# Optimization experiments

Measured on AMD Instinct MI355X. Metric: run time of the kernel, lower is better.

The kernel has to match this reference:

```python
import jax, jax.numpy as jnp
import numpy as np

H = 256  # hidden size


def _lstm_dir(x, w_ih, w_hh, b, reverse):
    """Single-direction LSTM. x: [B,S,D]; w_ih: [4H,D]; w_hh: [4H,H]; b: [4H].
    PyTorch gate order: i, f, g, o."""
    if reverse:
        x = jnp.flip(x, axis=1)
    # Precompute input contribution for all timesteps at once: [B,S,4H]
    xg = jnp.einsum('bsd,gd->bsg', x, w_ih) + b

    def step(carry, xg_t):
        h, c = carry
        gates = xg_t + h @ w_hh.T  # [B,4H]
        i, f, g, o = jnp.split(gates, 4, axis=-1)
        c = jax.nn.sigmoid(f) * c + jax.nn.sigmoid(i) * jnp.tanh(g)
        h = jax.nn.sigmoid(o) * jnp.tanh(c)
        return (h, c), h

    Bsz = x.shape[0]
    h0 = jnp.zeros((Bsz, w_hh.shape[1]), x.dtype)
    _, hs = jax.lax.scan(step, (h0, h0), jnp.swapaxes(xg, 0, 1))  # hs: [S,B,H]
    hs = jnp.swapaxes(hs, 0, 1)
    if reverse:
        hs = jnp.flip(hs, axis=1)
    return hs


def _bilstm_layer(x, w_ih, w_hh, b):
    # w_ih: [2,4H,D], w_hh: [2,4H,H], b: [2,4H] (b_ih + b_hh pre-summed)
    fwd = _lstm_dir(x, w_ih[0], w_hh[0], b[0], False)
    bwd = _lstm_dir(x, w_ih[1], w_hh[1], b[1], True)
    return jnp.concatenate([fwd, bwd], axis=-1)  # [B,S,2H]


def setup_inputs() -> dict:
    key = jax.random.key(0)
    ks = jax.random.split(key, 16)
    B, S, D = 256, 512, 64
    s = 1.0 / np.sqrt(H)
    u = lambda k, shp: jax.random.uniform(k, shp, jnp.float32, -s, s)
    return {
        'x': jax.random.normal(ks[0], (B, S, D), jnp.float32),
        # layer 0 (input D)
        'w_ih0': u(ks[1], (2, 4 * H, D)),
        'w_hh0': u(ks[2], (2, 4 * H, H)),
        'b0': u(ks[3], (2, 4 * H)),
        # layers 1..2 (input 2H)
        'w_ih_r': u(ks[4], (2, 2, 4 * H, 2 * H)),
        'w_hh_r': u(ks[5], (2, 2, 4 * H, H)),
        'b_r': u(ks[6], (2, 2, 4 * H)),
        # FC head: 2H -> H -> H//2 -> 1
        'fc1_w': u(ks[7], (H, 2 * H)),
        'fc1_b': u(ks[8], (H,)),
        'fc2_w': u(ks[9], (H // 2, H)),
        'fc2_b': u(ks[10], (H // 2,)),
        'fc3_w': u(ks[11], (1, H // 2)),
        'fc3_b': u(ks[12], (1,)),
    }


def reference(x, w_ih0, w_hh0, b0, w_ih_r, w_hh_r, b_r,
              fc1_w, fc1_b, fc2_w, fc2_b, fc3_w, fc3_b):
    h = _bilstm_layer(x, w_ih0, w_hh0, b0)
    for l in range(w_ih_r.shape[0]):  # fixed small layer count
        h = _bilstm_layer(h, w_ih_r[l], w_hh_r[l], b_r[l])
    last = h[:, -1, :]  # [B, 2H]
    h1 = jax.nn.relu(last @ fc1_w.T + fc1_b)
    h2 = jax.nn.relu(h1 @ fc2_w.T + fc2_b)
    return h2 @ fc3_w.T + fc3_b  # [B,1]
```

## Files before the change

kernel.cpp:

```cpp
#include <hip/hip_runtime.h>
#include <cstdint>
#include <cstddef>

#define B_ 256
#define S_ 512

typedef _Float16 f16;
typedef _Float16 f16x8 __attribute__((ext_vector_type(8)));
typedef _Float16 f16x4 __attribute__((ext_vector_type(4)));
typedef float f32x4 __attribute__((ext_vector_type(4)));
using u32 = unsigned int;
using u16 = unsigned short;
using u64 = unsigned long long;

#define TAGX   0x555u
#define MAGIC_ 0x13579BDFu

__device__ __forceinline__ float sigf(float x) { return 1.f / (1.f + __expf(-x)); }
__device__ __forceinline__ float tanh_f(float x) {
  x = fminf(15.f, fmaxf(-15.f, x));
  const float e = __expf(-2.f * x);
  return (1.f - e) / (1.f + e);
}
__device__ __forceinline__ f16x8 cvt_f16x8(float4 a, float4 b) {
  f16x8 t;
  t[0] = (f16)a.x; t[1] = (f16)a.y; t[2] = (f16)a.z; t[3] = (f16)a.w;
  t[4] = (f16)b.x; t[5] = (f16)b.y; t[6] = (f16)b.z; t[7] = (f16)b.w;
  return t;
}

__global__ __launch_bounds__(256) void transpose_x(
    const float* __restrict__ x, f16* __restrict__ xT)
{
  const int t = blockIdx.x;
  const int col = threadIdx.x & 63;
  const int r0 = threadIdx.x >> 6;
  for (int it = 0; it < 64; ++it) {
    const int row = (it << 2) + r0;
    xT[((size_t)t * 256 + row) * 64 + col] =
        (f16)x[((size_t)row * S_ + t) * 64 + col];
  }
}

template<int L, int KIN>
__global__ __launch_bounds__(256, 1) void lstm_layer(
    const f16* __restrict__ xT,
    f16* __restrict__ hA,
    f16* __restrict__ aux,
    f16* __restrict__ l2out,
    u64* __restrict__ exch,
    u32* __restrict__ xprog,
    const float* __restrict__ w_ih,
    const float* __restrict__ w_hh,
    const float* __restrict__ bias)
{
  constexpr int GPR = KIN / 8;
  constexpr int LG  = (KIN == 512) ? 6 : 3;
  constexpr int NG  = 16 * GPR;
  constexpr int XI  = (NG + 255) / 256;
  __shared__ __align__(16) f16 x_s[16 * KIN];
  __shared__ __align__(16) f16 h_s[16 * 256];
  __shared__ float gates_s[64 * 33];
  __shared__ char pad_[81920];

  const int tid = threadIdx.x;
  const int lane = tid & 63, w = tid >> 6;
  const int l15 = lane & 15, l4 = lane >> 4;
  const int phys = blockIdx.x;
  const int wg = ((phys & 7) << 5) | (phys >> 3);
  const int dirv = wg >> 7, bg = (wg >> 3) & 15, sl = wg & 7;
  if ((int)blockIdx.x == -1) { pad_[tid] = 0; }

  f16x8 bih[2][KIN / 32];
  f16x8 bhhH[2][8], bhhL[2][8];
#pragma unroll
  for (int nt = 0; nt < 2; ++nt) {
    const int grow = (w << 8) + (sl << 5) + (nt << 4) + l15;
    const float* pih = w_ih + ((size_t)(dirv << 10) + grow) * KIN + (l4 << 3);
#pragma unroll
    for (int kt = 0; kt < KIN / 32; ++kt) {
      const float* p = pih + (kt << 5);
      bih[nt][kt] = cvt_f16x8(*(const float4*)p, *(const float4*)(p + 4));
    }
    const float* phh = w_hh + ((size_t)(dirv << 10) + grow) * 256 + (l4 << 3);
#pragma unroll
    for (int kt = 0; kt < 8; ++kt) {
      const float* p = phh + (kt << 5);
      float wf[8];
      *(float4*)&wf[0] = *(const float4*)p;
      *(float4*)&wf[4] = *(const float4*)(p + 4);
      f16x8 hi, lo;
#pragma unroll
      for (int j = 0; j < 8; ++j) {
        hi[j] = (f16)wf[j];
        lo[j] = (f16)((wf[j] - (float)hi[j]) * 1024.f);
      }
      bhhH[nt][kt] = hi;
      bhhL[nt][kt] = lo;
    }
  }

  const int crow = tid >> 4;
  const int u0 = (tid & 15) << 1;
  float bv[4][2];
#pragma unroll
  for (int g = 0; g < 4; ++g)
#pragma unroll
    for (int j = 0; j < 2; ++j)
      bv[g][j] = bias[(dirv << 10) + (g << 8) + (sl << 5) + u0 + j];
  float cs0 = 0.f, cs1 = 0.f;

  auto xsrc = [&](int t, int b, int g) -> const f16* {
    if constexpr (L == 0) {
      return xT + ((size_t)t * 256 + b) * 64 + (g << 3);
    } else if constexpr (L == 1) {
      return hA + ((size_t)t * 256 + b) * 512 + (g << 3);
    } else {
      const int c0 = g << 3;
      if (c0 < 256)
        return (t < 256) ? aux + ((size_t)t * 256 + b) * 256 + c0
                         : hA + ((size_t)t * 256 + b) * 512 + c0;
      const int u = c0 - 256;
      return (t >= 256) ? aux + ((size_t)(256 + (511 - t)) * 256 + b) * 256 + u
                        : hA + ((size_t)t * 256 + b) * 512 + 256 + u;
    }
  };

#define X_MFMA(A0, A1)                                                         \
  {                                                                            \
    _Pragma("unroll")                                                          \
    for (int kt = 0; kt < KIN / 32; ++kt) {                                    \
      const int gg = ((kt << 2) + l4) ^ (l15 & 7);                             \
      const f16x8 a = *(const f16x8*)&x_s[l15 * KIN + (gg << 3)];              \
      A0 = __builtin_amdgcn_mfma_f32_16x16x32_f16(a, bih[0][kt], A0, 0, 0, 0); \
      A1 = __builtin_amdgcn_mfma_f32_16x16x32_f16(a, bih[1][kt], A1, 0, 0, 0); \
    }                                                                          \
  }

  f16x8 xreg[XI];
  {
    const int t0 = dirv ? (S_ - 1) : 0;
#pragma unroll
    for (int i = 0; i < XI; ++i) {
      const int G = tid + (i << 8);
      if (NG < 256 && G >= NG) break;
      const int row = G >> LG, g = G & (GPR - 1);
      xreg[i] = *(const f16x8*)xsrc(t0, (bg << 4) + row, g);
    }
#pragma unroll
    for (int i = 0; i < XI; ++i) {
      const int G = tid + (i << 8);
      if (NG < 256 && G >= NG) break;
      const int row = G >> LG, g = G & (GPR - 1);
      *(f16x8*)&x_s[row * KIN + ((g ^ (row & 7)) << 3)] = xreg[i];
    }
  }
  __syncthreads();
  f32x4 accx0 = {}, accx1 = {};
  X_MFMA(accx0, accx1);

  for (int s = 0; s < S_; ++s) {
    const int t_or = dirv ? (S_ - 1 - s) : s;
    const bool pf = (s + 1 < S_);

    if (pf) {
      const int t_nx = dirv ? (t_or - 1) : (t_or + 1);
#pragma unroll
      for (int i = 0; i < XI; ++i) {
        const int G = tid + (i << 8);
        if (NG < 256 && G >= NG) break;
        const int row = G >> LG, g = G & (GPR - 1);
        xreg[i] = *(const f16x8*)xsrc(t_nx, (bg << 4) + row, g);
      }
    }

    if constexpr (L == 1) {
      if (s == 256) {
        if (tid < 128) {
          const u32* pw = xprog + (1 - dirv) * 128 + tid;
          while (__hip_atomic_load(pw, __ATOMIC_RELAXED, __HIP_MEMORY_SCOPE_AGENT) != MAGIC_)
            __builtin_amdgcn_s_sleep(2);
        }
        __syncthreads();
      }
    }

    if (s > 0) {
      const u32 tagp = ((u32)(L * 512 + s - 1) ^ TAGX) & 0x7FFu;
      const u64* ex = exch + ((size_t)(((s - 1) & 1) * 2 + dirv)) * 256 * 128;
      u32 vv[4][4];
      for (;;) {
        bool ok = true;
#pragma unroll
        for (int i = 0; i < 4; ++i) {
          const int G = tid + (i << 8);
          const int row = G >> 6, gr = G & 63;
          const int b = (bg << 4) + row;
          const u64* p = ex + b * 128 + (gr << 1);
          const u64 a = __hip_atomic_load(p, __ATOMIC_RELAXED, __HIP_MEMORY_SCOPE_AGENT);
          const u64 c = __hip_atomic_load(p + 1, __ATOMIC_RELAXED, __HIP_MEMORY_SCOPE_AGENT);
          vv[i][0] = (u32)a; vv[i][1] = (u32)(a >> 32);
          vv[i][2] = (u32)c; vv[i][3] = (u32)(c >> 32);
#pragma unroll
          for (int j = 0; j < 4; ++j) ok &= ((vv[i][j] & 0x7FFu) == tagp);
        }
        if (ok) break;
        __builtin_amdgcn_s_sleep(1);
      }
#pragma unroll
      for (int i = 0; i < 4; ++i) {
        const int G = tid + (i << 8);
        const int row = G >> 6, gr = G & 63;
        const int g8 = gr >> 1, half = gr & 1;
        f16x4 hh;
#pragma unroll
        for (int j = 0; j < 4; ++j)
          hh[j] = (f16)__builtin_bit_cast(float, vv[i][j] & 0xFFFFF800u);
        *(f16x4*)&h_s[(row << 8) + ((g8 ^ (row & 7)) << 3) + (half << 2)] = hh;
      }
    }
    __syncthreads();

    f32x4 acc0 = accx0, acc1 = accx1;
    if (s > 0) {
      f32x4 aL0 = {}, aL1 = {};
#pragma unroll
      for (int kt = 0; kt < 8; ++kt) {
        const int gg = ((kt << 2) + l4) ^ (l15 & 7);
        const f16x8 a = *(const f16x8*)&h_s[(l15 << 8) + (gg << 3)];
        acc0 = __builtin_amdgcn_mfma_f32_16x16x32_f16(a, bhhH[0][kt], acc0, 0, 0, 0);
        acc1 = __builtin_amdgcn_mfma_f32_16x16x32_f16(a, bhhH[1][kt], acc1, 0, 0, 0);
        aL0 = __builtin_amdgcn_mfma_f32_16x16x32_f16(a, bhhL[0][kt], aL0, 0, 0, 0);
        aL1 = __builtin_amdgcn_mfma_f32_16x16x32_f16(a, bhhL[1][kt], aL1, 0, 0, 0);
      }
      acc0 += aL0 * (1.f / 1024.f);
      acc1 += aL1 * (1.f / 1024.f);
    }

#pragma unroll
    for (int r = 0; r < 4; ++r) {
      const int row = (l4 << 2) + r;
      gates_s[((w << 4) + row) * 33 + l15] = acc0[r];
      gates_s[((w << 4) + row) * 33 + 16 + l15] = acc1[r];
    }
    __syncthreads();

    float hv[2];
    {
      float css[2] = { cs0, cs1 };
#pragma unroll
      for (int j = 0; j < 2; ++j) {
        const int u = u0 + j;
        const float gi = gates_s[(0 * 16 + crow) * 33 + u] + bv[0][j];
        const float gf = gates_s[(1 * 16 + crow) * 33 + u] + bv[1][j];
        const float gg = gates_s[(2 * 16 + crow) * 33 + u] + bv[2][j];
        const float go = gates_s[(3 * 16 + crow) * 33 + u] + bv[3][j];
        float cc = sigf(gf) * css[j] + sigf(gi) * tanh_f(gg);
        css[j] = cc;
        hv[j] = sigf(go) * tanh_f(cc);
      }
      cs0 = css[0]; cs1 = css[1];
    }

    asm volatile("s_waitcnt vmcnt(0)" ::: "memory");
    {
      const u32 tagc = ((u32)(L * 512 + s) ^ TAGX) & 0x7FFu;
      const u32 w0 = ((__builtin_bit_cast(u32, hv[0]) + 0x400u) & 0xFFFFF800u) | tagc;
      const u32 w1 = ((__builtin_bit_cast(u32, hv[1]) + 0x400u) & 0xFFFFF800u) | tagc;
      const u64 pk = (u64)w0 | ((u64)w1 << 32);
      const int b = (bg << 4) + crow;
      __hip_atomic_store(
          exch + ((size_t)((s & 1) * 2 + dirv)) * 256 * 128 + b * 128 + (sl << 4) + (u0 >> 1),
          pk, __ATOMIC_RELAXED, __HIP_MEMORY_SCOPE_AGENT);

      union { u16 hw[2]; u32 pkh; } uh;
      uh.hw[0] = __builtin_bit_cast(u16, (f16)hv[0]);
      uh.hw[1] = __builtin_bit_cast(u16, (f16)hv[1]);
      const int uoff = (dirv << 7) + (sl << 4) + (u0 >> 1);
      if constexpr (L == 0) {
        ((u32*)hA)[((size_t)t_or * 256 + b) * 256 + uoff] = uh.pkh;
      } else if constexpr (L == 1) {
        if (s < 256)
          ((u32*)aux)[((size_t)(dirv * 256 + s) * 256 + b) * 128 + (sl << 4) + (u0 >> 1)] = uh.pkh;
        else
          ((u32*)hA)[((size_t)t_or * 256 + b) * 256 + uoff] = uh.pkh;
      } else {
        if (t_or == S_ - 1)
          ((u32*)l2out)[(size_t)b * 256 + uoff] = uh.pkh;
      }
    }

    if constexpr (L == 1) {
      if (s == 254) {
        asm volatile("s_waitcnt vmcnt(0)" ::: "memory");
        __syncthreads();
        if (tid == 0)
          __hip_atomic_store(xprog + dirv * 128 + (bg << 3) + sl, MAGIC_,
                             __ATOMIC_RELAXED, __HIP_MEMORY_SCOPE_AGENT);
      }
    }

    if (pf) {
#pragma unroll
      for (int i = 0; i < XI; ++i) {
        const int G = tid + (i << 8);
        if (NG < 256 && G >= NG) break;
        const int row = G >> LG, g = G & (GPR - 1);
        *(f16x8*)&x_s[row * KIN + ((g ^ (row & 7)) << 3)] = xreg[i];
      }
      __syncthreads();
      accx0 = (f32x4){}; accx1 = (f32x4){};
      X_MFMA(accx0, accx1);
    }
  }
#undef X_MFMA
}

__global__ __launch_bounds__(256) void fc_head(
    const f16* __restrict__ l2out,
    const float* __restrict__ fc1_w, const float* __restrict__ fc1_b,
    const float* __restrict__ fc2_w, const float* __restrict__ fc2_b,
    const float* __restrict__ fc3_w, const float* __restrict__ fc3_b,
    float* __restrict__ out)
{
  __shared__ float last[512];
  __shared__ float h1[256];
  __shared__ float h2[128];
  const int b = blockIdx.x;
  const int t = threadIdx.x;
  for (int i = t; i < 512; i += 256)
    last[i] = (float)l2out[(size_t)b * 512 + i];
  __syncthreads();
  {
    float a = fc1_b[t];
    for (int k = 0; k < 512; ++k) a = fmaf(last[k], fc1_w[t * 512 + k], a);
    h1[t] = fmaxf(a, 0.f);
  }
  __syncthreads();
  if (t < 128) {
    float a = fc2_b[t];
    for (int k = 0; k < 256; ++k) a = fmaf(h1[k], fc2_w[t * 256 + k], a);
    h2[t] = fmaxf(a, 0.f);
  }
  __syncthreads();
  if (t == 0) {
    float a = fc3_b[0];
    for (int k = 0; k < 128; ++k) a = fmaf(h2[k], fc3_w[k], a);
    out[b] = a;
  }
}

__global__ void sentinel(float* out, int n, float v) {
  const int i = blockIdx.x * blockDim.x + threadIdx.x;
  if (i < n) out[i] = v;
}

extern "C" void kernel_launch(void* const* d_in, const int* in_sizes, int n_in,
                              void* d_out, int out_size, void* d_ws, size_t ws_size,
                              hipStream_t stream) {
  (void)in_sizes; (void)n_in;
  const float* x      = (const float*)d_in[0];
  const float* w_ih0  = (const float*)d_in[1];
  const float* w_hh0  = (const float*)d_in[2];
  const float* b0     = (const float*)d_in[3];
  const float* w_ih_r = (const float*)d_in[4];
  const float* w_hh_r = (const float*)d_in[5];
  const float* b_r    = (const float*)d_in[6];
  const float* fc1_w  = (const float*)d_in[7];
  const float* fc1_b  = (const float*)d_in[8];
  const float* fc2_w  = (const float*)d_in[9];
  const float* fc2_b  = (const float*)d_in[10];
  const float* fc3_w  = (const float*)d_in[11];
  const float* fc3_b  = (const float*)d_in[12];
  float* out = (float*)d_out;

  const size_t off_hA    = 0;
  const size_t off_aux   = off_hA   + (size_t)512*256*512*2;
  const size_t off_xT    = off_aux  + (size_t)2*256*256*256*2;
  const size_t off_l2o   = off_xT   + (size_t)512*256*64*2;
  const size_t off_exch  = off_l2o  + (size_t)256*512*2;
  const size_t off_xprog = off_exch + (size_t)2*2*256*128*8;
  const size_t need      = off_xprog + 1024;
  if (ws_size < need) {
    sentinel<<<1, 256, 0, stream>>>(out, out_size, (float)(ws_size >> 20));
    return;
  }
  char* ws = (char*)d_ws;
  f16* hA    = (f16*)(ws + off_hA);
  f16* aux   = (f16*)(ws + off_aux);
  f16* xT    = (f16*)(ws + off_xT);
  f16* l2out = (f16*)(ws + off_l2o);
  u64* exch  = (u64*)(ws + off_exch);
  u32* xprog = (u32*)(ws + off_xprog);

  hipMemsetAsync(ws + off_exch, 0xAA, (size_t)2*2*256*128*8 + 1024, stream);

  transpose_x<<<512, 256, 0, stream>>>(x, xT);

  lstm_layer<0, 64><<<256, 256, 0, stream>>>(
      xT, hA, aux, l2out, exch, xprog, w_ih0, w_hh0, b0);
  lstm_layer<1, 512><<<256, 256, 0, stream>>>(
      xT, hA, aux, l2out, exch, xprog, w_ih_r, w_hh_r, b_r);
  lstm_layer<2, 512><<<256, 256, 0, stream>>>(
      xT, hA, aux, l2out, exch, xprog,
      w_ih_r + (size_t)2 * 1024 * 512, w_hh_r + (size_t)2 * 1024 * 256,
      b_r + 2048);

  fc_head<<<B_, 256, 0, stream>>>(l2out, fc1_w, fc1_b, fc2_w, fc2_b, fc3_w, fc3_b, out);
}
```

Measured before the change: 3.835 ms.

## Use 512-thread LSTM blocks covering 64 hidden units, halving the block count

Each persistent LSTM workgroup now has 8 waves and owns 64 hidden units instead of 32, so the grid drops from 256 to 128 blocks. Each thread now polls only the exchange words for its own h_s slot, with short spinning before it starts sleeping, and the per-step vmcnt(0) wait before publishing is dropped except near the layer-1 handoff. The aim is fewer blocks in the cross-block recurrence exchange and lower per-step sync latency. The cost is more MFMA and activation work per block, and the XCD/group mapping and progress-flag indexing had to be reworked.

```diff
diff --git a/kernel.cpp b/kernel.cpp
--- a/kernel.cpp
+++ b/kernel.cpp
@@ -7,7 +7,6 @@
 
 typedef _Float16 f16;
 typedef _Float16 f16x8 __attribute__((ext_vector_type(8)));
-typedef _Float16 f16x4 __attribute__((ext_vector_type(4)));
 typedef float f32x4 __attribute__((ext_vector_type(4)));
 using u32 = unsigned int;
 using u16 = unsigned short;
@@ -43,7 +42,7 @@
 }
 
 template<int L, int KIN>
-__global__ __launch_bounds__(256, 1) void lstm_layer(
+__global__ __launch_bounds__(512, 1) void lstm_layer(
     const f16* __restrict__ xT,
     f16* __restrict__ hA,
     f16* __restrict__ aux,
@@ -57,25 +56,29 @@
   constexpr int GPR = KIN / 8;
   constexpr int LG  = (KIN == 512) ? 6 : 3;
   constexpr int NG  = 16 * GPR;
-  constexpr int XI  = (NG + 255) / 256;
+  constexpr int XI  = (NG + 511) / 512;
   __shared__ __align__(16) f16 x_s[16 * KIN];
   __shared__ __align__(16) f16 h_s[16 * 256];
-  __shared__ float gates_s[64 * 33];
-  __shared__ char pad_[81920];
+  __shared__ float gates_s[64 * 66];
+  constexpr int PADB = 90112 - 16 * KIN * 2 - 16 * 256 * 2 - 64 * 66 * 4;
+  __shared__ char pad_[PADB];
 
   const int tid = threadIdx.x;
   const int lane = tid & 63, w = tid >> 6;
   const int l15 = lane & 15, l4 = lane >> 4;
+  const int gi = w >> 1, uh = w & 1;
   const int phys = blockIdx.x;
-  const int wg = ((phys & 7) << 5) | (phys >> 3);
-  const int dirv = wg >> 7, bg = (wg >> 3) & 15, sl = wg & 7;
-  if ((int)blockIdx.x == -1) { pad_[tid] = 0; }
+  const int xcd = phys & 7, slot = phys >> 3;
+  const int gp = slot >> 2, sl = slot & 3;
+  const int grp = (gp << 3) | xcd;
+  const int dirv = grp >> 4, bg = grp & 15;
+  if ((int)blockIdx.x == -1) pad_[tid] = 0;
 
   f16x8 bih[2][KIN / 32];
   f16x8 bhhH[2][8], bhhL[2][8];
 #pragma unroll
   for (int nt = 0; nt < 2; ++nt) {
-    const int grow = (w << 8) + (sl << 5) + (nt << 4) + l15;
+    const int grow = (gi << 8) + (sl << 6) + (uh << 5) + (nt << 4) + l15;
     const float* pih = w_ih + ((size_t)(dirv << 10) + grow) * KIN + (l4 << 3);
 #pragma unroll
     for (int kt = 0; kt < KIN / 32; ++kt) {
@@ -100,15 +103,16 @@
     }
   }
 
-  const int crow = tid >> 4;
-  const int u0 = (tid & 15) << 1;
+  const int crow = tid >> 5;
+  const int u0 = (tid & 31) << 1;
   float bv[4][2];
 #pragma unroll
   for (int g = 0; g < 4; ++g)
 #pragma unroll
     for (int j = 0; j < 2; ++j)
-      bv[g][j] = bias[(dirv << 10) + (g << 8) + (sl << 5) + u0 + j];
+      bv[g][j] = bias[(dirv << 10) + (g << 8) + (sl << 6) + u0 + j];
   float cs0 = 0.f, cs1 = 0.f;
+  const int sg8 = tid & 31;
 
   auto xsrc = [&](int t, int b, int g) -> const f16* {
     if constexpr (L == 0) {
@@ -142,15 +146,15 @@
     const int t0 = dirv ? (S_ - 1) : 0;
 #pragma unroll
     for (int i = 0; i < XI; ++i) {
-      const int G = tid + (i << 8);
-      if (NG < 256 && G >= NG) break;
+      const int G = tid + (i << 9);
+      if (NG < 512 && G >= NG) break;
       const int row = G >> LG, g = G & (GPR - 1);
       xreg[i] = *(const f16x8*)xsrc(t0, (bg << 4) + row, g);
     }
 #pragma unroll
     for (int i = 0; i < XI; ++i) {
-      const int G = tid + (i << 8);
-      if (NG < 256 && G >= NG) break;
+      const int G = tid + (i << 9);
+      if (NG < 512 && G >= NG) break;
       const int row = G >> LG, g = G & (GPR - 1);
       *(f16x8*)&x_s[row * KIN + ((g ^ (row & 7)) << 3)] = xreg[i];
     }
@@ -167,8 +171,8 @@
       const int t_nx = dirv ? (t_or - 1) : (t_or + 1);
 #pragma unroll
       for (int i = 0; i < XI; ++i) {
-        const int G = tid + (i << 8);
-        if (NG < 256 && G >= NG) break;
+        const int G = tid + (i << 9);
+        if (NG < 512 && G >= NG) break;
         const int row = G >> LG, g = G & (GPR - 1);
         xreg[i] = *(const f16x8*)xsrc(t_nx, (bg << 4) + row, g);
       }
@@ -176,8 +180,8 @@
 
     if constexpr (L == 1) {
       if (s == 256) {
-        if (tid < 128) {
-          const u32* pw = xprog + (1 - dirv) * 128 + tid;
+        if (tid < 64) {
+          const u32* pw = xprog + (1 - dirv) * 64 + tid;
           while (__hip_atomic_load(pw, __ATOMIC_RELAXED, __HIP_MEMORY_SCOPE_AGENT) != MAGIC_)
             __builtin_amdgcn_s_sleep(2);
         }
@@ -187,37 +191,27 @@
 
     if (s > 0) {
       const u32 tagp = ((u32)(L * 512 + s - 1) ^ TAGX) & 0x7FFu;
-      const u64* ex = exch + ((size_t)(((s - 1) & 1) * 2 + dirv)) * 256 * 128;
-      u32 vv[4][4];
-      for (;;) {
+      const u64* pb = exch + ((size_t)(((s - 1) & 1) * 2 + dirv)) * 256 * 128
+                      + ((bg << 4) + crow) * 128 + (sg8 << 2);
+      u64 a[4];
+      for (int tr = 0;; ++tr) {
+#pragma unroll
+        for (int k = 0; k < 4; ++k)
+          a[k] = __hip_atomic_load(pb + k, __ATOMIC_RELAXED, __HIP_MEMORY_SCOPE_AGENT);
         bool ok = true;
 #pragma unroll
-        for (int i = 0; i < 4; ++i) {
-          const int G = tid + (i << 8);
-          const int row = G >> 6, gr = G & 63;
-          const int b = (bg << 4) + row;
-          const u64* p = ex + b * 128 + (gr << 1);
-          const u64 a = __hip_atomic_load(p, __ATOMIC_RELAXED, __HIP_MEMORY_SCOPE_AGENT);
-          const u64 c = __hip_atomic_load(p + 1, __ATOMIC_RELAXED, __HIP_MEMORY_SCOPE_AGENT);
-          vv[i][0] = (u32)a; vv[i][1] = (u32)(a >> 32);
-          vv[i][2] = (u32)c; vv[i][3] = (u32)(c >> 32);
-#pragma unroll
-          for (int j = 0; j < 4; ++j) ok &= ((vv[i][j] & 0x7FFu) == tagp);
-        }
+        for (int k = 0; k < 4; ++k)
+          ok &= (((u32)a[k] & 0x7FFu) == tagp) & (((u32)(a[k] >> 32) & 0x7FFu) == tagp);
         if (ok) break;
-        __builtin_amdgcn_s_sleep(1);
-      }
-#pragma unroll
-      for (int i = 0; i < 4; ++i) {
-        const int G = tid + (i << 8);
-        const int row = G >> 6, gr = G & 63;
-        const int g8 = gr >> 1, half = gr & 1;
-        f16x4 hh;
-#pragma unroll
-        for (int j = 0; j < 4; ++j)
-          hh[j] = (f16)__builtin_bit_cast(float, vv[i][j] & 0xFFFFF800u);
-        *(f16x4*)&h_s[(row << 8) + ((g8 ^ (row & 7)) << 3) + (half << 2)] = hh;
-      }
+        if (tr >= 3) __builtin_amdgcn_s_sleep(1);
+      }
+      f16x8 hh;
+#pragma unroll
+      for (int k = 0; k < 4; ++k) {
+        hh[2 * k]     = (f16)__builtin_bit_cast(float, (u32)a[k] & 0xFFFFF800u);
+        hh[2 * k + 1] = (f16)__builtin_bit_cast(float, (u32)(a[k] >> 32) & 0xFFFFF800u);
+      }
+      *(f16x8*)&h_s[(crow << 8) + ((sg8 ^ (crow & 7)) << 3)] = hh;
     }
     __syncthreads();
 
@@ -240,8 +234,8 @@
 #pragma unroll
     for (int r = 0; r < 4; ++r) {
       const int row = (l4 << 2) + r;
-      gates_s[((w << 4) + row) * 33 + l15] = acc0[r];
-      gates_s[((w << 4) + row) * 33 + 16 + l15] = acc1[r];
+      gates_s[((gi << 4) + row) * 66 + (uh << 5) + l15] = acc0[r];
+      gates_s[((gi << 4) + row) * 66 + (uh << 5) + 16 + l15] = acc1[r];
     }
     __syncthreads();
 
@@ -251,42 +245,42 @@
 #pragma unroll
       for (int j = 0; j < 2; ++j) {
         const int u = u0 + j;
-        const float gi = gates_s[(0 * 16 + crow) * 33 + u] + bv[0][j];
-        const float gf = gates_s[(1 * 16 + crow) * 33 + u] + bv[1][j];
-        const float gg = gates_s[(2 * 16 + crow) * 33 + u] + bv[2][j];
-        const float go = gates_s[(3 * 16 + crow) * 33 + u] + bv[3][j];
-        float cc = sigf(gf) * css[j] + sigf(gi) * tanh_f(gg);
+        const float gI = gates_s[(0 * 16 + crow) * 66 + u] + bv[0][j];
+        const float gF = gates_s[(1 * 16 + crow) * 66 + u] + bv[1][j];
+        const float gG = gates_s[(2 * 16 + crow) * 66 + u] + bv[2][j];
+        const float gO = gates_s[(3 * 16 + crow) * 66 + u] + bv[3][j];
+        float cc = sigf(gF) * css[j] + sigf(gI) * tanh_f(gG);
         css[j] = cc;
-        hv[j] = sigf(go) * tanh_f(cc);
+        hv[j] = sigf(gO) * tanh_f(cc);
       }
       cs0 = css[0]; cs1 = css[1];
     }
 
-    asm volatile("s_waitcnt vmcnt(0)" ::: "memory");
+    if (L == 1 && s >= 253) asm volatile("s_waitcnt vmcnt(0)" ::: "memory");
     {
       const u32 tagc = ((u32)(L * 512 + s) ^ TAGX) & 0x7FFu;
       const u32 w0 = ((__builtin_bit_cast(u32, hv[0]) + 0x400u) & 0xFFFFF800u) | tagc;
       const u32 w1 = ((__builtin_bit_cast(u32, hv[1]) + 0x400u) & 0xFFFFF800u) | tagc;
       const u64 pk = (u64)w0 | ((u64)w1 << 32);
       const int b = (bg << 4) + crow;
-      __hip_atomic_store(
-          exch + ((size_t)((s & 1) * 2 + dirv)) * 256 * 128 + b * 128 + (sl << 4) + (u0 >> 1),
-          pk, __ATOMIC_RELAXED, __HIP_MEMORY_SCOPE_AGENT);
-
-      union { u16 hw[2]; u32 pkh; } uh;
-      uh.hw[0] = __builtin_bit_cast(u16, (f16)hv[0]);
-      uh.hw[1] = __builtin_bit_cast(u16, (f16)hv[1]);
-      const int uoff = (dirv << 7) + (sl << 4) + (u0 >> 1);
+      const size_t eidx = ((size_t)((s & 1) * 2 + dirv)) * 256 * 128
+                          + b * 128 + (sl << 5) + (u0 >> 1);
+      __hip_atomic_store(exch + eidx, pk, __ATOMIC_RELAXED, __HIP_MEMORY_SCOPE_AGENT);
+
+      union { u16 hw[2]; u32 pkh; } uhh;
+      uhh.hw[0] = __builtin_bit_cast(u16, (f16)hv[0]);
+      uhh.hw[1] = __builtin_bit_cast(u16, (f16)hv[1]);
+      const int uoff = (dirv << 7) + (sl << 5) + (u0 >> 1);
       if constexpr (L == 0) {
-        ((u32*)hA)[((size_t)t_or * 256 + b) * 256 + uoff] = uh.pkh;
+        ((u32*)hA)[((size_t)t_or * 256 + b) * 256 + uoff] = uhh.pkh;
       } else if constexpr (L == 1) {
         if (s < 256)
-          ((u32*)aux)[((size_t)(dirv * 256 + s) * 256 + b) * 128 + (sl << 4) + (u0 >> 1)] = uh.pkh;
+          ((u32*)aux)[((size_t)(dirv * 256 + s) * 256 + b) * 128 + (sl << 5) + (u0 >> 1)] = uhh.pkh;
         else
-          ((u32*)hA)[((size_t)t_or * 256 + b) * 256 + uoff] = uh.pkh;
+          ((u32*)hA)[((size_t)t_or * 256 + b) * 256 + uoff] = uhh.pkh;
       } else {
         if (t_or == S_ - 1)
-          ((u32*)l2out)[(size_t)b * 256 + uoff] = uh.pkh;
+          ((u32*)l2out)[(size_t)b * 256 + uoff] = uhh.pkh;
       }
     }
 
@@ -295,7 +289,7 @@
         asm volatile("s_waitcnt vmcnt(0)" ::: "memory");
         __syncthreads();
         if (tid == 0)
-          __hip_atomic_store(xprog + dirv * 128 + (bg << 3) + sl, MAGIC_,
+          __hip_atomic_store(xprog + dirv * 64 + (bg << 2) + sl, MAGIC_,
                              __ATOMIC_RELAXED, __HIP_MEMORY_SCOPE_AGENT);
       }
     }
@@ -303,8 +297,8 @@
     if (pf) {
 #pragma unroll
       for (int i = 0; i < XI; ++i) {
-        const int G = tid + (i << 8);
-        if (NG < 256 && G >= NG) break;
+        const int G = tid + (i << 9);
+        if (NG < 512 && G >= NG) break;
         const int row = G >> LG, g = G & (GPR - 1);
         *(f16x8*)&x_s[row * KIN + ((g ^ (row & 7)) << 3)] = xreg[i];
       }
@@ -375,11 +369,11 @@
   float* out = (float*)d_out;
 
   const size_t off_hA    = 0;
-  const size_t off_aux   = off_hA   + (size_t)512*256*512*2;
-  const size_t off_xT    = off_aux  + (size_t)2*256*256*256*2;
-  const size_t off_l2o   = off_xT   + (size_t)512*256*64*2;
-  const size_t off_exch  = off_l2o  + (size_t)256*512*2;
-  const size_t off_xprog = off_exch + (size_t)2*2*256*128*8;
+  const size_t off_aux   = off_hA    + (size_t)512*256*512*2;
+  const size_t off_xT    = off_aux   + (size_t)2*256*256*256*2;
+  const size_t off_l2o   = off_xT    + (size_t)512*256*64*2;
+  const size_t off_exch  = off_l2o   + (size_t)256*512*2;
+  const size_t off_xprog = off_exch  + (size_t)2*2*256*128*8;
   const size_t need      = off_xprog + 1024;
   if (ws_size < need) {
     sentinel<<<1, 256, 0, stream>>>(out, out_size, (float)(ws_size >> 20));
@@ -397,11 +391,11 @@
 
   transpose_x<<<512, 256, 0, stream>>>(x, xT);
 
-  lstm_layer<0, 64><<<256, 256, 0, stream>>>(
+  lstm_layer<0, 64><<<128, 512, 0, stream>>>(
       xT, hA, aux, l2out, exch, xprog, w_ih0, w_hh0, b0);
-  lstm_layer<1, 512><<<256, 256, 0, stream>>>(
+  lstm_layer<1, 512><<<128, 512, 0, stream>>>(
       xT, hA, aux, l2out, exch, xprog, w_ih_r, w_hh_r, b_r);
-  lstm_layer<2, 512><<<256, 256, 0, stream>>>(
+  lstm_layer<2, 512><<<128, 512, 0, stream>>>(
       xT, hA, aux, l2out, exch, xprog,
       w_ih_r + (size_t)2 * 1024 * 512, w_hh_r + (size_t)2 * 1024 * 256,
       b_r + 2048);
```

Measured after the change: 11.02 ms. 187% more time.

## Permute gate rows so LSTM cell update runs in registers via lane shuffles

Applied to the files above, without the earlier changes.

Reorders the weight rows each wave loads so that every lane's MFMA accumulators hold the i/f/g/o gate values for the same hidden units. A lane-xor-8 shuffle then pairs them, so the cell update runs directly from registers. This removes the LDS gates buffer and one __syncthreads per timestep. Output packing also uses lane-xor-1 shuffles, and the per-step s_waitcnt vmcnt(0) is now issued only near the layer-1 handoff step. The costs are more shuffle instructions, redundant transcendental work on half the lanes, and a looser wait on outstanding stores.

```diff
diff --git a/kernel.cpp b/kernel.cpp
--- a/kernel.cpp
+++ b/kernel.cpp
@@ -60,7 +60,6 @@
   constexpr int XI  = (NG + 255) / 256;
   __shared__ __align__(16) f16 x_s[16 * KIN];
   __shared__ __align__(16) f16 h_s[16 * 256];
-  __shared__ float gates_s[64 * 33];
   __shared__ char pad_[81920];
 
   const int tid = threadIdx.x;
@@ -69,13 +68,16 @@
   const int phys = blockIdx.x;
   const int wg = ((phys & 7) << 5) | (phys >> 3);
   const int dirv = wg >> 7, bg = (wg >> 3) & 15, sl = wg & 7;
-  if ((int)blockIdx.x == -1) { pad_[tid] = 0; }
+  if ((int)blockIdx.x == -1) pad_[tid] = 0;
 
   f16x8 bih[2][KIN / 32];
   f16x8 bhhH[2][8], bhhL[2][8];
+  float bv[2];
 #pragma unroll
   for (int nt = 0; nt < 2; ++nt) {
-    const int grow = (w << 8) + (sl << 5) + (nt << 4) + l15;
+    const int g_gate = (nt << 1) + (l15 >> 3);
+    const int grow = (g_gate << 8) + (sl << 5) + (w << 3) + (l15 & 7);
+    bv[nt] = bias[(dirv << 10) + grow];
     const float* pih = w_ih + ((size_t)(dirv << 10) + grow) * KIN + (l4 << 3);
 #pragma unroll
     for (int kt = 0; kt < KIN / 32; ++kt) {
@@ -100,15 +102,7 @@
     }
   }
 
-  const int crow = tid >> 4;
-  const int u0 = (tid & 15) << 1;
-  float bv[4][2];
-#pragma unroll
-  for (int g = 0; g < 4; ++g)
-#pragma unroll
-    for (int j = 0; j < 2; ++j)
-      bv[g][j] = bias[(dirv << 10) + (g << 8) + (sl << 5) + u0 + j];
-  float cs0 = 0.f, cs1 = 0.f;
+  float cs[4] = {0.f, 0.f, 0.f, 0.f};
 
   auto xsrc = [&](int t, int b, int g) -> const f16* {
     if constexpr (L == 0) {
@@ -187,7 +181,7 @@
 
     if (s > 0) {
       const u32 tagp = ((u32)(L * 512 + s - 1) ^ TAGX) & 0x7FFu;
-      const u64* ex = exch + ((size_t)(((s - 1) & 1) * 2 + dirv)) * 256 * 128;
+      const size_t ebase = ((size_t)(((s - 1) & 1) * 2 + dirv)) * 256 * 128;
       u32 vv[4][4];
       for (;;) {
         bool ok = true;
@@ -195,8 +189,7 @@
         for (int i = 0; i < 4; ++i) {
           const int G = tid + (i << 8);
           const int row = G >> 6, gr = G & 63;
-          const int b = (bg << 4) + row;
-          const u64* p = ex + b * 128 + (gr << 1);
+          const u64* p = exch + ebase + ((bg << 4) + row) * 128 + (gr << 1);
           const u64 a = __hip_atomic_load(p, __ATOMIC_RELAXED, __HIP_MEMORY_SCOPE_AGENT);
           const u64 c = __hip_atomic_load(p + 1, __ATOMIC_RELAXED, __HIP_MEMORY_SCOPE_AGENT);
           vv[i][0] = (u32)a; vv[i][1] = (u32)(a >> 32);
@@ -237,56 +230,57 @@
       acc1 += aL1 * (1.f / 1024.f);
     }
 
-#pragma unroll
-    for (int r = 0; r < 4; ++r) {
-      const int row = (l4 << 2) + r;
-      gates_s[((w << 4) + row) * 33 + l15] = acc0[r];
-      gates_s[((w << 4) + row) * 33 + 16 + l15] = acc1[r];
-    }
-    __syncthreads();
-
-    float hv[2];
+    float hv[4];
     {
-      float css[2] = { cs0, cs1 };
-#pragma unroll
-      for (int j = 0; j < 2; ++j) {
-        const int u = u0 + j;
-        const float gi = gates_s[(0 * 16 + crow) * 33 + u] + bv[0][j];
-        const float gf = gates_s[(1 * 16 + crow) * 33 + u] + bv[1][j];
-        const float gg = gates_s[(2 * 16 + crow) * 33 + u] + bv[2][j];
-        const float go = gates_s[(3 * 16 + crow) * 33 + u] + bv[3][j];
-        float cc = sigf(gf) * css[j] + sigf(gi) * tanh_f(gg);
-        css[j] = cc;
-        hv[j] = sigf(go) * tanh_f(cc);
-      }
-      cs0 = css[0]; cs1 = css[1];
-    }
-
-    asm volatile("s_waitcnt vmcnt(0)" ::: "memory");
+      const bool loH = (l15 < 8);
+#pragma unroll
+      for (int r = 0; r < 4; ++r) {
+        const float a0 = acc0[r] + bv[0];
+        const float a1 = acc1[r] + bv[1];
+        const float o0 = __shfl_xor(a0, 8);
+        const float o1 = __shfl_xor(a1, 8);
+        const float gi = loH ? a0 : o0;
+        const float gf = loH ? o0 : a0;
+        const float gg = loH ? a1 : o1;
+        const float go = loH ? o1 : a1;
+        float cc = sigf(gf) * cs[r] + sigf(gi) * tanh_f(gg);
+        cs[r] = cc;
+        hv[r] = sigf(go) * tanh_f(cc);
+      }
+    }
+
+    if (L == 1 && s >= 253) asm volatile("s_waitcnt vmcnt(0)" ::: "memory");
     {
       const u32 tagc = ((u32)(L * 512 + s) ^ TAGX) & 0x7FFu;
-      const u32 w0 = ((__builtin_bit_cast(u32, hv[0]) + 0x400u) & 0xFFFFF800u) | tagc;
-      const u32 w1 = ((__builtin_bit_cast(u32, hv[1]) + 0x400u) & 0xFFFFF800u) | tagc;
-      const u64 pk = (u64)w0 | ((u64)w1 << 32);
-      const int b = (bg << 4) + crow;
-      __hip_atomic_store(
-          exch + ((size_t)((s & 1) * 2 + dirv)) * 256 * 128 + b * 128 + (sl << 4) + (u0 >> 1),
-          pk, __ATOMIC_RELAXED, __HIP_MEMORY_SCOPE_AGENT);
-
-      union { u16 hw[2]; u32 pkh; } uh;
-      uh.hw[0] = __builtin_bit_cast(u16, (f16)hv[0]);
-      uh.hw[1] = __builtin_bit_cast(u16, (f16)hv[1]);
-      const int uoff = (dirv << 7) + (sl << 4) + (u0 >> 1);
-      if constexpr (L == 0) {
-        ((u32*)hA)[((size_t)t_or * 256 + b) * 256 + uoff] = uh.pkh;
-      } else if constexpr (L == 1) {
-        if (s < 256)
-          ((u32*)aux)[((size_t)(dirv * 256 + s) * 256 + b) * 128 + (sl << 4) + (u0 >> 1)] = uh.pkh;
-        else
-          ((u32*)hA)[((size_t)t_or * 256 + b) * 256 + uoff] = uh.pkh;
-      } else {
-        if (t_or == S_ - 1)
-          ((u32*)l2out)[(size_t)b * 256 + uoff] = uh.pkh;
+      const size_t pbase = ((size_t)((s & 1) * 2 + dirv)) * 256 * 128;
+      const int p_g = (sl << 4) + (w << 2) + ((l15 & 7) >> 1);
+      const bool evenL = ((l15 & 1) == 0);
+      const int rhalf = (l15 >> 3) << 1;
+#pragma unroll
+      for (int r = 0; r < 4; ++r) {
+        const u32 tw = ((__builtin_bit_cast(u32, hv[r]) + 0x400u) & 0xFFFFF800u) | tagc;
+        const u32 nb = __shfl_xor(tw, 1);
+        const u32 h16 = (u32)__builtin_bit_cast(u16, (f16)hv[r]);
+        const u32 nh = __shfl_xor(h16, 1);
+        if (evenL && (r == rhalf || r == rhalf + 1)) {
+          const u64 pk64 = (u64)tw | ((u64)nb << 32);
+          const u32 pkh = h16 | (nh << 16);
+          const int b = (bg << 4) + (l4 << 2) + r;
+          __hip_atomic_store(exch + pbase + (size_t)b * 128 + p_g, pk64,
+                             __ATOMIC_RELAXED, __HIP_MEMORY_SCOPE_AGENT);
+          const int uoff = (dirv << 7) + p_g;
+          if constexpr (L == 0) {
+            ((u32*)hA)[((size_t)t_or * 256 + b) * 256 + uoff] = pkh;
+          } else if constexpr (L == 1) {
+            if (s < 256)
+              ((u32*)aux)[((size_t)(dirv * 256 + s) * 256 + b) * 128 + p_g] = pkh;
+            else
+              ((u32*)hA)[((size_t)t_or * 256 + b) * 256 + uoff] = pkh;
+          } else {
+            if (t_or == S_ - 1)
+              ((u32*)l2out)[(size_t)b * 256 + uoff] = pkh;
+          }
+        }
       }
     }
 
@@ -375,11 +369,11 @@
   float* out = (float*)d_out;
 
   const size_t off_hA    = 0;
-  const size_t off_aux   = off_hA   + (size_t)512*256*512*2;
-  const size_t off_xT    = off_aux  + (size_t)2*256*256*256*2;
-  const size_t off_l2o   = off_xT   + (size_t)512*256*64*2;
-  const size_t off_exch  = off_l2o  + (size_t)256*512*2;
-  const size_t off_xprog = off_exch + (size_t)2*2*256*128*8;
+  const size_t off_aux   = off_hA    + (size_t)512*256*512*2;
+  const size_t off_xT    = off_aux   + (size_t)2*256*256*256*2;
+  const size_t off_l2o   = off_xT    + (size_t)512*256*64*2;
+  const size_t off_exch  = off_l2o   + (size_t)256*512*2;
+  const size_t off_xprog = off_exch  + (size_t)2*2*256*128*8;
   const size_t need      = off_xprog + 1024;
   if (ws_size < need) {
     sentinel<<<1, 256, 0, stream>>>(out, out_size, (float)(ws_size >> 20));
```

After: 5.118 ms. +33.4%, slower.
